# Kernel tuning notes

Measured on AMD Instinct MI355X. Metric: run time of the kernel, lower is better.

Reference implementation:

```python
import jax, jax.numpy as jnp
import numpy as np

B, T, D = 2, 2048, 2048   # batch, seq, model dim
H = 1408                  # expert hidden dim
E = 16                    # routed experts
S = 2                     # shared experts
TOP_K = 2
SCALE = 0.02


def setup_inputs() -> dict:
    key = jax.random.key(0)
    ks = jax.random.split(key, 6)
    return {
        "x": jax.random.normal(ks[0], (B, T, D), jnp.float32),
        "gate_w": jax.random.normal(ks[1], (D, E), jnp.float32) * SCALE,
        "shared_w1": jax.random.normal(ks[2], (S, D, H), jnp.float32) * SCALE,
        "shared_w2": jax.random.normal(ks[3], (S, H, D), jnp.float32) * SCALE,
        "expert_w1": jax.random.normal(ks[4], (E, D, H), jnp.float32) * SCALE,
        "expert_w2": jax.random.normal(ks[5], (E, H, D), jnp.float32) * SCALE,
    }


def reference(x, gate_w, shared_w1, shared_w2, expert_w1, expert_w2):
    xf = x.reshape(-1, x.shape[-1])            # [T_tot, D]
    n_tok = xf.shape[0]

    # shared experts: sum of SiLU FFNs
    sh = jax.nn.silu(jnp.einsum('td,sdh->sth', xf, shared_w1))
    shared_out = jnp.einsum('sth,shd->td', sh, shared_w2)

    # router
    logits = xf @ gate_w                       # [T_tot, E]
    probs = jax.nn.softmax(logits, axis=-1)
    topk_w, topk_idx = jax.lax.top_k(probs, TOP_K)
    topk_w = topk_w / topk_w.sum(axis=-1, keepdims=True)

    # aux load-balancing loss
    aux_loss = (probs.mean(axis=0) * logits.mean(axis=0)).sum() * E

    # scatter normalized top-k weights into dense [T_tot, E] combine matrix
    combine = jnp.zeros((n_tok, E), xf.dtype).at[
        jnp.arange(n_tok)[:, None], topk_idx
    ].add(topk_w)

    # routed experts computed densely over all tokens, combined by routing weights
    h = jax.nn.silu(jnp.einsum('td,edh->eth', xf, expert_w1))   # [E, T_tot, H]
    eo = jnp.einsum('eth,ehd->etd', h, expert_w2)               # [E, T_tot, D]
    routed_out = jnp.einsum('te,etd->td', combine, eo)

    total = (shared_out + routed_out).reshape(x.shape)
    return total, aux_loss
```

## Files before the change

kernel.cpp:

```cpp
#include <hip/hip_runtime.h>
#include <hip/hip_bf16.h>


#define T_TOT   4096
#define DMODEL  2048
#define HDIM    1408
#define NEXP    16
#define MAXSLOT 10240
#define MAXTILE 80

typedef short     bf16x8_t  __attribute__((ext_vector_type(8)));
typedef float     f32x4_t   __attribute__((ext_vector_type(4)));
typedef ushort    u16x8_t   __attribute__((ext_vector_type(8)));

__device__ __forceinline__ ushort f2bf(float f) {
    unsigned u = __float_as_uint(f);
    u += 0x7fffu + ((u >> 16) & 1u);
    return (ushort)(u >> 16);
}
__device__ __forceinline__ float bf2f(ushort b) { return __uint_as_float((unsigned)b << 16); }
__device__ __forceinline__ float silu(float v) { return v / (1.0f + __expf(-v)); }

__device__ __forceinline__ void async16(const ushort* g, ushort* l) {
    __builtin_amdgcn_global_load_lds((const __attribute__((address_space(1))) void*)g,
                                     (__attribute__((address_space(3))) void*)l, 16, 0, 0);
}


__global__ void init_kernel(int* cnt, double* ps, double* ls) {
    if (threadIdx.x < NEXP) { cnt[threadIdx.x] = 0; ps[threadIdx.x] = 0.0; ls[threadIdx.x] = 0.0; }
}

__global__ __launch_bounds__(256) void cvt_bf16(const float* __restrict__ src, ushort* __restrict__ dst) {
    size_t i = ((size_t)blockIdx.x * 256 + threadIdx.x) * 4;
    float4 v = *(const float4*)(src + i);
    ushort4 o; o.x = f2bf(v.x); o.y = f2bf(v.y); o.z = f2bf(v.z); o.w = f2bf(v.w);
    *(ushort4*)(dst + i) = o;
}

__global__ __launch_bounds__(256) void transpose_cvt(const float* __restrict__ src, ushort* __restrict__ dst,
                                                     int R, int C, long sbatch, long dbatch, int ldd) {
    __shared__ ushort t[64][72];
    const float* s = src + (long)blockIdx.z * sbatch;
    ushort* d = dst + (long)blockIdx.z * dbatch;
    int c0 = blockIdx.x * 64, r0 = blockIdx.y * 64;
    int tx = threadIdx.x & 15, ty = threadIdx.x >> 4;
#pragma unroll
    for (int i = 0; i < 4; i++) {
        int r = ty + i * 16;
        float4 v = *(const float4*)(s + (size_t)(r0 + r) * C + c0 + tx * 4);
        ushort4 o; o.x = f2bf(v.x); o.y = f2bf(v.y); o.z = f2bf(v.z); o.w = f2bf(v.w);
        *(ushort4*)&t[r][tx * 4] = o;
    }
    __syncthreads();
    int cx = threadIdx.x & 7, cy = threadIdx.x >> 3;
#pragma unroll
    for (int i = 0; i < 2; i++) {
        int cc = cy + i * 32;
        u16x8_t o;
#pragma unroll
        for (int j = 0; j < 8; j++) o[j] = t[cx * 8 + j][cc];
        *(u16x8_t*)(d + (size_t)(c0 + cc) * ldd + r0 + cx * 8) = o;
    }
}


__global__ __launch_bounds__(256) void router_kernel(const float* __restrict__ x, const float* __restrict__ gw,
                                                     int* __restrict__ topk_idx, float* __restrict__ topk_w,
                                                     double* __restrict__ probs_sum, double* __restrict__ logits_sum,
                                                     int* __restrict__ cnt) {
    const int wv = threadIdx.x >> 6, l = threadIdx.x & 63;
    const int tBase = blockIdx.x * 8 + wv * 2;

    float acc0[NEXP], acc1[NEXP];
#pragma unroll
    for (int e = 0; e < NEXP; e++) { acc0[e] = 0.f; acc1[e] = 0.f; }

    const float* x0 = x + (size_t)tBase * DMODEL;
    const float* x1 = x0 + DMODEL;

#pragma unroll
    for (int i = 0; i < 8; i++) {
        const int d0 = i * 256 + l * 4;
        float4 xa = *(const float4*)(x0 + d0);
        float4 xb = *(const float4*)(x1 + d0);
        const float4* g = (const float4*)(gw + (size_t)d0 * NEXP);
        float gf[64];
#pragma unroll
        for (int j = 0; j < 16; j++) {
            float4 t = g[j];
            gf[4 * j] = t.x; gf[4 * j + 1] = t.y; gf[4 * j + 2] = t.z; gf[4 * j + 3] = t.w;
        }
        const float xs0[4] = {xa.x, xa.y, xa.z, xa.w};
        const float xs1[4] = {xb.x, xb.y, xb.z, xb.w};
#pragma unroll
        for (int r = 0; r < 4; r++)
#pragma unroll
            for (int e = 0; e < NEXP; e++) {
                acc0[e] += xs0[r] * gf[r * 16 + e];
                acc1[e] += xs1[r] * gf[r * 16 + e];
            }
    }

#pragma unroll
    for (int e = 0; e < NEXP; e++) {
        acc0[e] += __shfl_xor(acc0[e], 32); acc0[e] += __shfl_xor(acc0[e], 16);
        acc1[e] += __shfl_xor(acc1[e], 32); acc1[e] += __shfl_xor(acc1[e], 16);
    }

    __shared__ float  sred[4][2][16][17];
    __shared__ double sp[4][2][NEXP], sl[4][2][NEXP];

    if (l < 16) {
#pragma unroll
        for (int e = 0; e < NEXP; e++) { sred[wv][0][l][e] = acc0[e]; sred[wv][1][l][e] = acc1[e]; }
    }
    __syncthreads();

    if (l < 32) {
        const int tok = l >> 4, e = l & 15;
        double lg = 0.0;
#pragma unroll
        for (int g = 0; g < 16; g++) lg += (double)sred[wv][tok][g][e];

        double m = lg;
#pragma unroll
        for (int off = 8; off; off >>= 1) { double o = __shfl_xor(m, off); m = o > m ? o : m; }
        double pe = exp(lg - m);
        double ss = pe;
#pragma unroll
        for (int off = 8; off; off >>= 1) ss += __shfl_xor(ss, off);
        double p = pe / ss;

        double v = p; int ie = e;
#pragma unroll
        for (int off = 8; off; off >>= 1) {
            double ov = __shfl_xor(v, off); int oi = __shfl_xor(ie, off);
            if (ov > v || (ov == v && oi < ie)) { v = ov; ie = oi; }
        }
        double v2 = (e == ie) ? -1.0 : p; int ie2 = e;
#pragma unroll
        for (int off = 8; off; off >>= 1) {
            double ov = __shfl_xor(v2, off); int oi = __shfl_xor(ie2, off);
            if (ov > v2 || (ov == v2 && oi < ie2)) { v2 = ov; ie2 = oi; }
        }

        sp[wv][tok][e] = p; sl[wv][tok][e] = lg;

        if (e == 0) {
            int t = tBase + tok;
            double s2 = v + v2;
            topk_idx[t * 2] = ie;  topk_idx[t * 2 + 1] = ie2;
            topk_w[t * 2] = (float)(v / s2); topk_w[t * 2 + 1] = (float)(v2 / s2);
            atomicAdd(&cnt[ie], 1); atomicAdd(&cnt[ie2], 1);
        }
    }
    __syncthreads();

    if (threadIdx.x < NEXP) {
        int e = threadIdx.x;
        double ps = 0.0, ls = 0.0;
#pragma unroll
        for (int w = 0; w < 4; w++) { ps += sp[w][0][e] + sp[w][1][e]; ls += sl[w][0][e] + sl[w][1][e]; }
        atomicAdd(&probs_sum[e], ps); atomicAdd(&logits_sum[e], ls);
    }
}

__global__ void setup_kernel(const int* __restrict__ cnt, int* __restrict__ cursor,
                             int* __restrict__ tile_expert, int* __restrict__ tile_row, int* __restrict__ meta,
                             int* __restrict__ slot_token, float* __restrict__ slot_w,
                             const double* __restrict__ probs_sum, const double* __restrict__ logits_sum,
                             float* __restrict__ out_aux) {
    if (threadIdx.x == 0) {
        int off = 0, nt = 0;
        for (int e = 0; e < NEXP; e++) {
            cursor[e] = off;
            int tiles = (cnt[e] + 127) >> 7;
            for (int j = 0; j < tiles; j++) { tile_expert[nt] = e; tile_row[nt] = off + j * 128; nt++; }
            off += tiles * 128;
        }
        meta[0] = nt; meta[1] = off;
        double aux = 0.0;
        for (int e = 0; e < NEXP; e++)
            aux += (probs_sum[e] / (double)T_TOT) * (logits_sum[e] / (double)T_TOT);
        out_aux[0] = (float)(aux * (double)NEXP);
    }
    __syncthreads();
    for (int i = threadIdx.x; i < MAXSLOT; i += 256) { slot_token[i] = 0; slot_w[i] = 0.0f; }
}

__global__ void scatter_kernel(const int* __restrict__ topk_idx, const float* __restrict__ topk_w,
                               int* __restrict__ cursor, int* __restrict__ slot_token, float* __restrict__ slot_w,
                               int* __restrict__ slot_of) {
    int t = blockIdx.x * 256 + threadIdx.x;
#pragma unroll
    for (int k = 0; k < 2; k++) {
        int e = topk_idx[t * 2 + k];
        int pos = atomicAdd(&cursor[e], 1);
        slot_token[pos] = t;
        slot_w[pos] = topk_w[t * 2 + k];
        slot_of[t * 2 + k] = pos;
    }
}


template<bool INDIRECT_A>
__device__ __forceinline__ void gemm_tile_core(const ushort* __restrict__ A, const ushort* __restrict__ B,
                                               int lda, int ldb, int K, int m0, int n0,
                                               const int* __restrict__ rowmap,
                                               f32x4_t acc[4][4], ushort* lds) {
    const int tid = threadIdx.x;
    const int w = tid >> 6, l = tid & 63;
    const int c0 = w * 2, c1 = c0 + 1;
    const int subrow = l >> 2;
    const int kc = (l & 3) * 8;
    int ar0 = c0 * 16 + subrow, ar1 = c1 * 16 + subrow;
    long ga0, ga1;
    if (INDIRECT_A) { ga0 = (long)rowmap[m0 + ar0]; ga1 = (long)rowmap[m0 + ar1]; }
    else            { ga0 = (long)(m0 + ar0);       ga1 = (long)(m0 + ar1); }
    const ushort* pa0 = A + ga0 * lda + kc;
    const ushort* pa1 = A + ga1 * lda + kc;
    const ushort* pb0 = B + (long)(n0 + ar0) * ldb + kc;
    const ushort* pb1 = B + (long)(n0 + ar1) * ldb + kc;
    const int wm = w & 1, wn = w >> 1;
    const int lrow = l & 15, quad = l >> 4;

    {
        ushort* d0 = lds + c0 * 512;
        ushort* d1 = lds + c1 * 512;
        async16(pa0, d0); async16(pa1, d1);
        async16(pb0, d0 + 4096); async16(pb1, d1 + 4096);
    }
    int cur = 0;
    for (int kt = 0; kt < K; kt += 32) {
        __syncthreads();
        if (kt + 32 < K) {
            pa0 += 32; pa1 += 32; pb0 += 32; pb1 += 32;
            ushort* e0 = lds + (cur ^ 1) * 8192 + c0 * 512;
            ushort* e1 = lds + (cur ^ 1) * 8192 + c1 * 512;
            async16(pa0, e0); async16(pa1, e1);
            async16(pb0, e0 + 4096); async16(pb1, e1 + 4096);
        }
        const ushort* As = lds + cur * 8192;
        const ushort* Bs = As + 4096;
        bf16x8_t a[4], b[4];
#pragma unroll
        for (int mi = 0; mi < 4; mi++)
            a[mi] = *(const bf16x8_t*)(As + (wm * 64 + mi * 16 + lrow) * 32 + quad * 8);
#pragma unroll
        for (int ni = 0; ni < 4; ni++)
            b[ni] = *(const bf16x8_t*)(Bs + (wn * 64 + ni * 16 + lrow) * 32 + quad * 8);
#pragma unroll
        for (int mi = 0; mi < 4; mi++)
#pragma unroll
            for (int ni = 0; ni < 4; ni++)
                acc[mi][ni] = __builtin_amdgcn_mfma_f32_16x16x32_bf16(a[mi], b[ni], acc[mi][ni], 0, 0, 0);
        cur ^= 1;
    }
}

template<int MODE>
__global__ __launch_bounds__(256, 3) void gemm_dense(const ushort* __restrict__ A, const ushort* __restrict__ B,
                                                     void* __restrict__ C, int lda, int ldb, int ldc, int K,
                                                     long bStride, int cZOff) {
    __shared__ ushort lds[16384];
    int m0 = blockIdx.x * 128, n0 = blockIdx.y * 128;
    const ushort* Bz = B + (long)blockIdx.z * bStride;
    f32x4_t acc[4][4];
#pragma unroll
    for (int mi = 0; mi < 4; mi++)
#pragma unroll
        for (int ni = 0; ni < 4; ni++) acc[mi][ni] = (f32x4_t){0.f, 0.f, 0.f, 0.f};
    gemm_tile_core<false>(A, Bz, lda, ldb, K, m0, n0, nullptr, acc, lds);

    const int w = threadIdx.x >> 6, l = threadIdx.x & 63;
    const int wm = w & 1, wn = w >> 1, quad = l >> 4, lcol = l & 15;
    int colBase = (int)blockIdx.z * cZOff + n0 + wn * 64;
#pragma unroll
    for (int mi = 0; mi < 4; mi++) {
        int rowb = m0 + wm * 64 + mi * 16 + quad * 4;
#pragma unroll
        for (int ni = 0; ni < 4; ni++) {
            int col = colBase + ni * 16 + lcol;
#pragma unroll
            for (int r = 0; r < 4; r++) {
                float v = acc[mi][ni][r];
                if (MODE == 0) ((ushort*)C)[(long)(rowb + r) * ldc + col] = f2bf(silu(v));
                else           ((float*)C)[(long)(rowb + r) * ldc + col] = v;
            }
        }
    }
}

template<int MODE>
__global__ __launch_bounds__(256, 3) void gemm_grouped(const ushort* __restrict__ A, const ushort* __restrict__ B,
                                                       void* __restrict__ C, int lda, int ldb, int ldc, int K,
                                                       long bExpertStride,
                                                       const int* __restrict__ tile_expert,
                                                       const int* __restrict__ tile_row,
                                                       const int* __restrict__ meta,
                                                       const int* __restrict__ slot_token,
                                                       const float* __restrict__ slot_w) {
    if ((int)blockIdx.x >= meta[0]) return;
    __shared__ ushort lds[16384];
    int e = tile_expert[blockIdx.x];
    int m0 = tile_row[blockIdx.x];
    int n0 = blockIdx.y * 128;
    const ushort* Be = B + (long)e * bExpertStride;
    f32x4_t acc[4][4];
#pragma unroll
    for (int mi = 0; mi < 4; mi++)
#pragma unroll
        for (int ni = 0; ni < 4; ni++) acc[mi][ni] = (f32x4_t){0.f, 0.f, 0.f, 0.f};
    gemm_tile_core<MODE == 1>(A, Be, lda, ldb, K, m0, n0, slot_token, acc, lds);

    const int w = threadIdx.x >> 6, l = threadIdx.x & 63;
    const int wm = w & 1, wn = w >> 1, quad = l >> 4, lcol = l & 15;
#pragma unroll
    for (int mi = 0; mi < 4; mi++) {
        int rowb = m0 + wm * 64 + mi * 16 + quad * 4;
#pragma unroll
        for (int ni = 0; ni < 4; ni++) {
            int col = n0 + wn * 64 + ni * 16 + lcol;
#pragma unroll
            for (int r = 0; r < 4; r++) {
                float v = acc[mi][ni][r];
                int row = rowb + r;
                if (MODE == 1) {
                    ((ushort*)C)[(long)row * ldc + col] = f2bf(silu(v));
                } else {
                    float wt = slot_w[row];
                    ((ushort*)C)[(long)row * ldc + col] = f2bf(v * wt);
                }
            }
        }
    }
}

__global__ __launch_bounds__(256) void combine_kernel(float* __restrict__ out, const ushort* __restrict__ ro,
                                                      const int* __restrict__ slot_of) {
    int t = blockIdx.x;
    int s1 = slot_of[t * 2], s2 = slot_of[t * 2 + 1];
    const u16x8_t* r1 = (const u16x8_t*)(ro + (size_t)s1 * DMODEL);
    const u16x8_t* r2 = (const u16x8_t*)(ro + (size_t)s2 * DMODEL);
    int i = threadIdx.x;
    u16x8_t a = r1[i], b = r2[i];
    float4* o = (float4*)(out + (size_t)t * DMODEL) + i * 2;
    float4 o0 = o[0], o1 = o[1];
    o0.x += bf2f(a[0]) + bf2f(b[0]); o0.y += bf2f(a[1]) + bf2f(b[1]);
    o0.z += bf2f(a[2]) + bf2f(b[2]); o0.w += bf2f(a[3]) + bf2f(b[3]);
    o1.x += bf2f(a[4]) + bf2f(b[4]); o1.y += bf2f(a[5]) + bf2f(b[5]);
    o1.z += bf2f(a[6]) + bf2f(b[6]); o1.w += bf2f(a[7]) + bf2f(b[7]);
    o[0] = o0; o[1] = o1;
}


extern "C" void kernel_launch(void* const* d_in, const int* in_sizes, int n_in,
                              void* d_out, int out_size, void* d_ws, size_t ws_size,
                              hipStream_t stream) {
    const float* x   = (const float*)d_in[0];
    const float* gw  = (const float*)d_in[1];
    const float* sw1 = (const float*)d_in[2];
    const float* sw2 = (const float*)d_in[3];
    const float* ew1 = (const float*)d_in[4];
    const float* ew2 = (const float*)d_in[5];
    float* out = (float*)d_out;

    char* p = (char*)d_ws;
    auto alloc = [&](size_t bytes) { char* r = p; p += (bytes + 511) & ~(size_t)511; return r; };
    ushort* xb    = (ushort*)alloc((size_t)T_TOT * DMODEL * 2);
    ushort* w1t   = (ushort*)alloc((size_t)2 * HDIM * DMODEL * 2);
    ushort* w2t   = (ushort*)alloc((size_t)DMODEL * 2 * HDIM * 2);
    ushort* ew1t  = (ushort*)alloc((size_t)NEXP * HDIM * DMODEL * 2);
    ushort* ew2t  = (ushort*)alloc((size_t)NEXP * DMODEL * HDIM * 2);
    ushort* h     = (ushort*)alloc((size_t)T_TOT * 2 * HDIM * 2);
    ushort* hg    = (ushort*)alloc((size_t)MAXSLOT * HDIM * 2);
    ushort* ro    = (ushort*)alloc((size_t)MAXSLOT * DMODEL * 2);
    int*    slot_token = (int*)alloc(MAXSLOT * 4);
    float*  slot_w     = (float*)alloc(MAXSLOT * 4);
    int*    slot_of    = (int*)alloc(T_TOT * 2 * 4);
    int*    topk_idx   = (int*)alloc(T_TOT * 2 * 4);
    float*  topk_w     = (float*)alloc(T_TOT * 2 * 4);
    int*    cnt        = (int*)alloc(64);
    int*    cursor     = (int*)alloc(64);
    int*    tile_expert= (int*)alloc(512);
    int*    tile_row   = (int*)alloc(512);
    int*    meta       = (int*)alloc(64);
    double* probs_sum  = (double*)alloc(128);
    double* logits_sum = (double*)alloc(128);

    init_kernel<<<1, 64, 0, stream>>>(cnt, probs_sum, logits_sum);
    cvt_bf16<<<(T_TOT * DMODEL) / 1024, 256, 0, stream>>>(x, xb);
    transpose_cvt<<<dim3(HDIM / 64, DMODEL / 64, 2), 256, 0, stream>>>(
        sw1, w1t, DMODEL, HDIM, (long)DMODEL * HDIM, (long)HDIM * DMODEL, DMODEL);
    transpose_cvt<<<dim3(DMODEL / 64, HDIM / 64, 2), 256, 0, stream>>>(
        sw2, w2t, HDIM, DMODEL, (long)HDIM * DMODEL, (long)HDIM, 2 * HDIM);
    transpose_cvt<<<dim3(HDIM / 64, DMODEL / 64, NEXP), 256, 0, stream>>>(
        ew1, ew1t, DMODEL, HDIM, (long)DMODEL * HDIM, (long)HDIM * DMODEL, DMODEL);
    transpose_cvt<<<dim3(DMODEL / 64, HDIM / 64, NEXP), 256, 0, stream>>>(
        ew2, ew2t, HDIM, DMODEL, (long)HDIM * DMODEL, (long)DMODEL * HDIM, HDIM);

    router_kernel<<<T_TOT / 8, 256, 0, stream>>>(x, gw, topk_idx, topk_w, probs_sum, logits_sum, cnt);
    setup_kernel<<<1, 256, 0, stream>>>(cnt, cursor, tile_expert, tile_row, meta,
                                        slot_token, slot_w, probs_sum, logits_sum, out + (size_t)T_TOT * DMODEL);
    scatter_kernel<<<T_TOT / 256, 256, 0, stream>>>(topk_idx, topk_w, cursor, slot_token, slot_w, slot_of);

    gemm_dense<0><<<dim3(T_TOT / 128, HDIM / 128, 2), 256, 0, stream>>>(
        xb, w1t, h, DMODEL, DMODEL, 2 * HDIM, DMODEL, (long)HDIM * DMODEL, HDIM);
    gemm_grouped<1><<<dim3(MAXTILE, HDIM / 128), 256, 0, stream>>>(
        xb, ew1t, hg, DMODEL, DMODEL, HDIM, DMODEL, (long)HDIM * DMODEL,
        tile_expert, tile_row, meta, slot_token, slot_w);
    gemm_dense<2><<<dim3(T_TOT / 128, DMODEL / 128, 1), 256, 0, stream>>>(
        h, w2t, out, 2 * HDIM, 2 * HDIM, DMODEL, 2 * HDIM, 0L, 0);
    gemm_grouped<3><<<dim3(MAXTILE, DMODEL / 128), 256, 0, stream>>>(
        hg, ew2t, ro, HDIM, HDIM, DMODEL, HDIM, (long)DMODEL * HDIM,
        tile_expert, tile_row, meta, slot_token, slot_w);
    combine_kernel<<<T_TOT, 256, 0, stream>>>(out, ro, slot_of);
}
```

Measured before the change: 914.0 us.

## Merge prep, routing-plan and GEMM launches into fewer combined kernels

Collapses the conversion, transpose, router, setup and scatter kernels into one prep kernel plus a single-block plan kernel. The x-to-bf16 conversion is folded into the router, and router statistics are written as per-block partials instead of global atomics. The dense shared-expert GEMM and the grouped expert GEMM are merged into one launch per layer, so both run in the same grid and fill the GPU better. This saves launch overhead and tail idle time, but adds a serial single-block plan step that handles histogram, zeroing and scatter.

```diff
diff --git a/kernel.cpp b/kernel.cpp
--- a/kernel.cpp
+++ b/kernel.cpp
@@ -8,6 +8,7 @@
 #define NEXP    16
 #define MAXSLOT 10240
 #define MAXTILE 80
+#define RBLK    512
 
 typedef short     bf16x8_t  __attribute__((ext_vector_type(8)));
 typedef float     f32x4_t   __attribute__((ext_vector_type(4)));
@@ -27,30 +28,30 @@
 }
 
 
-__global__ void init_kernel(int* cnt, double* ps, double* ls) {
-    if (threadIdx.x < NEXP) { cnt[threadIdx.x] = 0; ps[threadIdx.x] = 0.0; ls[threadIdx.x] = 0.0; }
-}
-
-__global__ __launch_bounds__(256) void cvt_bf16(const float* __restrict__ src, ushort* __restrict__ dst) {
-    size_t i = ((size_t)blockIdx.x * 256 + threadIdx.x) * 4;
-    float4 v = *(const float4*)(src + i);
-    ushort4 o; o.x = f2bf(v.x); o.y = f2bf(v.y); o.z = f2bf(v.z); o.w = f2bf(v.w);
-    *(ushort4*)(dst + i) = o;
-}
-
-__global__ __launch_bounds__(256) void transpose_cvt(const float* __restrict__ src, ushort* __restrict__ dst,
-                                                     int R, int C, long sbatch, long dbatch, int ldd) {
-    __shared__ ushort t[64][72];
-    const float* s = src + (long)blockIdx.z * sbatch;
-    ushort* d = dst + (long)blockIdx.z * dbatch;
-    int c0 = blockIdx.x * 64, r0 = blockIdx.y * 64;
+union SMem {
+    struct {
+        float  sred[4][2][16][17];
+        double sp[4][2][NEXP];
+        double sl[4][2][NEXP];
+    } r;
+    ushort t[64][72];
+};
+
+__device__ __forceinline__ void transpose_tile(SMem& sm, int id,
+        const float* __restrict__ src, ushort* __restrict__ dst,
+        int C, long sbatch, long dbatch, int ldd, int TX, int TY) {
+    int z = id / (TX * TY); int rem = id - z * TX * TY;
+    int bx = rem % TX, by = rem / TX;
+    const float* s = src + (long)z * sbatch;
+    ushort* d = dst + (long)z * dbatch;
+    int c0 = bx * 64, r0 = by * 64;
     int tx = threadIdx.x & 15, ty = threadIdx.x >> 4;
 #pragma unroll
     for (int i = 0; i < 4; i++) {
         int r = ty + i * 16;
         float4 v = *(const float4*)(s + (size_t)(r0 + r) * C + c0 + tx * 4);
         ushort4 o; o.x = f2bf(v.x); o.y = f2bf(v.y); o.z = f2bf(v.z); o.w = f2bf(v.w);
-        *(ushort4*)&t[r][tx * 4] = o;
+        *(ushort4*)&sm.t[r][tx * 4] = o;
     }
     __syncthreads();
     int cx = threadIdx.x & 7, cy = threadIdx.x >> 3;
@@ -59,18 +60,17 @@
         int cc = cy + i * 32;
         u16x8_t o;
 #pragma unroll
-        for (int j = 0; j < 8; j++) o[j] = t[cx * 8 + j][cc];
+        for (int j = 0; j < 8; j++) o[j] = sm.t[cx * 8 + j][cc];
         *(u16x8_t*)(d + (size_t)(c0 + cc) * ldd + r0 + cx * 8) = o;
     }
 }
 
-
-__global__ __launch_bounds__(256) void router_kernel(const float* __restrict__ x, const float* __restrict__ gw,
-                                                     int* __restrict__ topk_idx, float* __restrict__ topk_w,
-                                                     double* __restrict__ probs_sum, double* __restrict__ logits_sum,
-                                                     int* __restrict__ cnt) {
+__device__ __forceinline__ void router_block(SMem& sm, int bid,
+        const float* __restrict__ x, const float* __restrict__ gw, ushort* __restrict__ xbuf,
+        int* __restrict__ topk_idx, float* __restrict__ topk_w,
+        double* __restrict__ pparts, double* __restrict__ lparts) {
     const int wv = threadIdx.x >> 6, l = threadIdx.x & 63;
-    const int tBase = blockIdx.x * 8 + wv * 2;
+    const int tBase = bid * 8 + wv * 2;
 
     float acc0[NEXP], acc1[NEXP];
 #pragma unroll
@@ -78,28 +78,32 @@
 
     const float* x0 = x + (size_t)tBase * DMODEL;
     const float* x1 = x0 + DMODEL;
+    ushort* xo0 = xbuf + (size_t)tBase * DMODEL;
+    ushort* xo1 = xo0 + DMODEL;
 
 #pragma unroll
     for (int i = 0; i < 8; i++) {
         const int d0 = i * 256 + l * 4;
         float4 xa = *(const float4*)(x0 + d0);
-        float4 xb = *(const float4*)(x1 + d0);
-        const float4* g = (const float4*)(gw + (size_t)d0 * NEXP);
-        float gf[64];
-#pragma unroll
-        for (int j = 0; j < 16; j++) {
-            float4 t = g[j];
-            gf[4 * j] = t.x; gf[4 * j + 1] = t.y; gf[4 * j + 2] = t.z; gf[4 * j + 3] = t.w;
-        }
+        float4 xb4 = *(const float4*)(x1 + d0);
+        ushort4 oa; oa.x = f2bf(xa.x); oa.y = f2bf(xa.y); oa.z = f2bf(xa.z); oa.w = f2bf(xa.w);
+        ushort4 ob; ob.x = f2bf(xb4.x); ob.y = f2bf(xb4.y); ob.z = f2bf(xb4.z); ob.w = f2bf(xb4.w);
+        *(ushort4*)(xo0 + d0) = oa;
+        *(ushort4*)(xo1 + d0) = ob;
         const float xs0[4] = {xa.x, xa.y, xa.z, xa.w};
-        const float xs1[4] = {xb.x, xb.y, xb.z, xb.w};
-#pragma unroll
-        for (int r = 0; r < 4; r++)
+        const float xs1[4] = {xb4.x, xb4.y, xb4.z, xb4.w};
+#pragma unroll
+        for (int r = 0; r < 4; r++) {
+            const float4* g = (const float4*)(gw + (size_t)(d0 + r) * NEXP);
+            float4 q0 = g[0], q1 = g[1], q2 = g[2], q3 = g[3];
+            const float gf[16] = {q0.x, q0.y, q0.z, q0.w, q1.x, q1.y, q1.z, q1.w,
+                                  q2.x, q2.y, q2.z, q2.w, q3.x, q3.y, q3.z, q3.w};
 #pragma unroll
             for (int e = 0; e < NEXP; e++) {
-                acc0[e] += xs0[r] * gf[r * 16 + e];
-                acc1[e] += xs1[r] * gf[r * 16 + e];
+                acc0[e] += xs0[r] * gf[e];
+                acc1[e] += xs1[r] * gf[e];
             }
+        }
     }
 
 #pragma unroll
@@ -108,12 +112,9 @@
         acc1[e] += __shfl_xor(acc1[e], 32); acc1[e] += __shfl_xor(acc1[e], 16);
     }
 
-    __shared__ float  sred[4][2][16][17];
-    __shared__ double sp[4][2][NEXP], sl[4][2][NEXP];
-
     if (l < 16) {
 #pragma unroll
-        for (int e = 0; e < NEXP; e++) { sred[wv][0][l][e] = acc0[e]; sred[wv][1][l][e] = acc1[e]; }
+        for (int e = 0; e < NEXP; e++) { sm.r.sred[wv][0][l][e] = acc0[e]; sm.r.sred[wv][1][l][e] = acc1[e]; }
     }
     __syncthreads();
 
@@ -121,7 +122,7 @@
         const int tok = l >> 4, e = l & 15;
         double lg = 0.0;
 #pragma unroll
-        for (int g = 0; g < 16; g++) lg += (double)sred[wv][tok][g][e];
+        for (int g = 0; g < 16; g++) lg += (double)sm.r.sred[wv][tok][g][e];
 
         double m = lg;
 #pragma unroll
@@ -145,14 +146,13 @@
             if (ov > v2 || (ov == v2 && oi < ie2)) { v2 = ov; ie2 = oi; }
         }
 
-        sp[wv][tok][e] = p; sl[wv][tok][e] = lg;
+        sm.r.sp[wv][tok][e] = p; sm.r.sl[wv][tok][e] = lg;
 
         if (e == 0) {
             int t = tBase + tok;
             double s2 = v + v2;
             topk_idx[t * 2] = ie;  topk_idx[t * 2 + 1] = ie2;
             topk_w[t * 2] = (float)(v / s2); topk_w[t * 2 + 1] = (float)(v2 / s2);
-            atomicAdd(&cnt[ie], 1); atomicAdd(&cnt[ie2], 1);
         }
     }
     __syncthreads();
@@ -161,45 +161,95 @@
         int e = threadIdx.x;
         double ps = 0.0, ls = 0.0;
 #pragma unroll
-        for (int w = 0; w < 4; w++) { ps += sp[w][0][e] + sp[w][1][e]; ls += sl[w][0][e] + sl[w][1][e]; }
-        atomicAdd(&probs_sum[e], ps); atomicAdd(&logits_sum[e], ls);
-    }
-}
-
-__global__ void setup_kernel(const int* __restrict__ cnt, int* __restrict__ cursor,
-                             int* __restrict__ tile_expert, int* __restrict__ tile_row, int* __restrict__ meta,
-                             int* __restrict__ slot_token, float* __restrict__ slot_w,
-                             const double* __restrict__ probs_sum, const double* __restrict__ logits_sum,
-                             float* __restrict__ out_aux) {
-    if (threadIdx.x == 0) {
+        for (int w = 0; w < 4; w++) { ps += sm.r.sp[w][0][e] + sm.r.sp[w][1][e]; ls += sm.r.sl[w][0][e] + sm.r.sl[w][1][e]; }
+        pparts[bid * NEXP + e] = ps;
+        lparts[bid * NEXP + e] = ls;
+    }
+}
+
+#define PB0 RBLK
+#define PB1 (PB0 + 1408)
+#define PB2 (PB1 + 1408)
+#define PB3 (PB2 + 11264)
+#define PB4 (PB3 + 11264)
+
+__global__ __launch_bounds__(256) void prep_kernel(
+        const float* __restrict__ x, const float* __restrict__ gw,
+        const float* __restrict__ sw1, const float* __restrict__ sw2,
+        const float* __restrict__ ew1, const float* __restrict__ ew2,
+        ushort* __restrict__ xb, ushort* __restrict__ w1t, ushort* __restrict__ w2t,
+        ushort* __restrict__ ew1t, ushort* __restrict__ ew2t,
+        int* __restrict__ topk_idx, float* __restrict__ topk_w,
+        double* __restrict__ pparts, double* __restrict__ lparts) {
+    __shared__ SMem sm;
+    int bid = blockIdx.x;
+    if (bid < PB0) {
+        router_block(sm, bid, x, gw, xb, topk_idx, topk_w, pparts, lparts);
+    } else if (bid < PB1) {
+        transpose_tile(sm, bid - PB0, sw1, w1t, HDIM, (long)DMODEL * HDIM, (long)HDIM * DMODEL,
+                       DMODEL, HDIM / 64, DMODEL / 64);
+    } else if (bid < PB2) {
+        transpose_tile(sm, bid - PB1, sw2, w2t, DMODEL, (long)HDIM * DMODEL, (long)HDIM,
+                       2 * HDIM, DMODEL / 64, HDIM / 64);
+    } else if (bid < PB3) {
+        transpose_tile(sm, bid - PB2, ew1, ew1t, HDIM, (long)DMODEL * HDIM, (long)HDIM * DMODEL,
+                       DMODEL, HDIM / 64, DMODEL / 64);
+    } else {
+        transpose_tile(sm, bid - PB3, ew2, ew2t, DMODEL, (long)HDIM * DMODEL, (long)DMODEL * HDIM,
+                       HDIM, DMODEL / 64, HDIM / 64);
+    }
+}
+
+
+__global__ __launch_bounds__(1024) void plan_kernel(
+        const int* __restrict__ topk_idx, const float* __restrict__ topk_w,
+        const double* __restrict__ pparts, const double* __restrict__ lparts,
+        int* __restrict__ tile_expert, int* __restrict__ tile_row, int* __restrict__ meta,
+        int* __restrict__ slot_token, float* __restrict__ slot_w, int* __restrict__ slot_of,
+        float* __restrict__ out_aux) {
+    __shared__ int hist[NEXP];
+    __shared__ int curs[NEXP];
+    __shared__ double pred[32][NEXP], lred[32][NEXP];
+    __shared__ double paux[NEXP], laux[NEXP];
+    const int tid = threadIdx.x;
+    if (tid < NEXP) hist[tid] = 0;
+    __syncthreads();
+    for (int i = tid; i < T_TOT * 2; i += 1024) atomicAdd(&hist[topk_idx[i]], 1);
+    for (int i = tid; i < MAXSLOT; i += 1024) { slot_token[i] = 0; slot_w[i] = 0.0f; }
+    if (tid < 512) {
+        int e = tid & 15, c = tid >> 4;
+        double ps = 0.0, ls = 0.0;
+        for (int b = c * 16; b < c * 16 + 16; b++) { ps += pparts[b * NEXP + e]; ls += lparts[b * NEXP + e]; }
+        pred[c][e] = ps; lred[c][e] = ls;
+    }
+    __syncthreads();
+    if (tid < NEXP) {
+        double ps = 0.0, ls = 0.0;
+        for (int c = 0; c < 32; c++) { ps += pred[c][tid]; ls += lred[c][tid]; }
+        paux[tid] = ps; laux[tid] = ls;
+    }
+    __syncthreads();
+    if (tid == 0) {
         int off = 0, nt = 0;
         for (int e = 0; e < NEXP; e++) {
-            cursor[e] = off;
-            int tiles = (cnt[e] + 127) >> 7;
+            curs[e] = off;
+            int tiles = (hist[e] + 127) >> 7;
             for (int j = 0; j < tiles; j++) { tile_expert[nt] = e; tile_row[nt] = off + j * 128; nt++; }
             off += tiles * 128;
         }
         meta[0] = nt; meta[1] = off;
         double aux = 0.0;
         for (int e = 0; e < NEXP; e++)
-            aux += (probs_sum[e] / (double)T_TOT) * (logits_sum[e] / (double)T_TOT);
+            aux += (paux[e] / (double)T_TOT) * (laux[e] / (double)T_TOT);
         out_aux[0] = (float)(aux * (double)NEXP);
     }
     __syncthreads();
-    for (int i = threadIdx.x; i < MAXSLOT; i += 256) { slot_token[i] = 0; slot_w[i] = 0.0f; }
-}
-
-__global__ void scatter_kernel(const int* __restrict__ topk_idx, const float* __restrict__ topk_w,
-                               int* __restrict__ cursor, int* __restrict__ slot_token, float* __restrict__ slot_w,
-                               int* __restrict__ slot_of) {
-    int t = blockIdx.x * 256 + threadIdx.x;
-#pragma unroll
-    for (int k = 0; k < 2; k++) {
-        int e = topk_idx[t * 2 + k];
-        int pos = atomicAdd(&cursor[e], 1);
-        slot_token[pos] = t;
-        slot_w[pos] = topk_w[t * 2 + k];
-        slot_of[t * 2 + k] = pos;
+    for (int i = tid; i < T_TOT * 2; i += 1024) {
+        int e = topk_idx[i];
+        int pos = atomicAdd(&curs[e], 1);
+        slot_token[pos] = i >> 1;
+        slot_w[pos] = topk_w[i];
+        slot_of[i] = pos;
     }
 }
 
@@ -259,78 +309,98 @@
     }
 }
 
-template<int MODE>
-__global__ __launch_bounds__(256, 3) void gemm_dense(const ushort* __restrict__ A, const ushort* __restrict__ B,
-                                                     void* __restrict__ C, int lda, int ldb, int ldc, int K,
-                                                     long bStride, int cZOff) {
+__global__ __launch_bounds__(256, 3) void gemm_p1(const ushort* __restrict__ xb,
+        const ushort* __restrict__ w1t, const ushort* __restrict__ ew1t,
+        ushort* __restrict__ h, ushort* __restrict__ hg,
+        const int* __restrict__ tile_expert, const int* __restrict__ tile_row,
+        const int* __restrict__ meta, const int* __restrict__ slot_token) {
     __shared__ ushort lds[16384];
-    int m0 = blockIdx.x * 128, n0 = blockIdx.y * 128;
-    const ushort* Bz = B + (long)blockIdx.z * bStride;
     f32x4_t acc[4][4];
 #pragma unroll
     for (int mi = 0; mi < 4; mi++)
 #pragma unroll
         for (int ni = 0; ni < 4; ni++) acc[mi][ni] = (f32x4_t){0.f, 0.f, 0.f, 0.f};
-    gemm_tile_core<false>(A, Bz, lda, ldb, K, m0, n0, nullptr, acc, lds);
+
+    const int bid = blockIdx.x;
+    ushort* C; int ldc, m0, n0, colBase;
+    if (bid < 704) {
+        int z = bid / 352, rem = bid % 352;
+        m0 = (rem % 32) * 128; n0 = (rem / 32) * 128;
+        gemm_tile_core<false>(xb, w1t + (long)z * HDIM * DMODEL, DMODEL, DMODEL, DMODEL,
+                              m0, n0, nullptr, acc, lds);
+        C = h; ldc = 2 * HDIM; colBase = z * HDIM + n0;
+    } else {
+        int r = bid - 704;
+        int tile = r % MAXTILE; n0 = (r / MAXTILE) * 128;
+        if (tile >= meta[0]) return;
+        int e = tile_expert[tile]; m0 = tile_row[tile];
+        gemm_tile_core<true>(xb, ew1t + (long)e * HDIM * DMODEL, DMODEL, DMODEL, DMODEL,
+                             m0, n0, slot_token, acc, lds);
+        C = hg; ldc = HDIM; colBase = n0;
+    }
 
     const int w = threadIdx.x >> 6, l = threadIdx.x & 63;
     const int wm = w & 1, wn = w >> 1, quad = l >> 4, lcol = l & 15;
-    int colBase = (int)blockIdx.z * cZOff + n0 + wn * 64;
 #pragma unroll
     for (int mi = 0; mi < 4; mi++) {
         int rowb = m0 + wm * 64 + mi * 16 + quad * 4;
 #pragma unroll
         for (int ni = 0; ni < 4; ni++) {
-            int col = colBase + ni * 16 + lcol;
-#pragma unroll
-            for (int r = 0; r < 4; r++) {
-                float v = acc[mi][ni][r];
-                if (MODE == 0) ((ushort*)C)[(long)(rowb + r) * ldc + col] = f2bf(silu(v));
-                else           ((float*)C)[(long)(rowb + r) * ldc + col] = v;
-            }
-        }
-    }
-}
-
-template<int MODE>
-__global__ __launch_bounds__(256, 3) void gemm_grouped(const ushort* __restrict__ A, const ushort* __restrict__ B,
-                                                       void* __restrict__ C, int lda, int ldb, int ldc, int K,
-                                                       long bExpertStride,
-                                                       const int* __restrict__ tile_expert,
-                                                       const int* __restrict__ tile_row,
-                                                       const int* __restrict__ meta,
-                                                       const int* __restrict__ slot_token,
-                                                       const float* __restrict__ slot_w) {
-    if ((int)blockIdx.x >= meta[0]) return;
+            int col = colBase + wn * 64 + ni * 16 + lcol;
+#pragma unroll
+            for (int r = 0; r < 4; r++)
+                C[(long)(rowb + r) * ldc + col] = f2bf(silu(acc[mi][ni][r]));
+        }
+    }
+}
+
+__global__ __launch_bounds__(256, 3) void gemm_p2(const ushort* __restrict__ h,
+        const ushort* __restrict__ w2t, const ushort* __restrict__ hg, const ushort* __restrict__ ew2t,
+        float* __restrict__ out, ushort* __restrict__ ro,
+        const int* __restrict__ tile_expert, const int* __restrict__ tile_row,
+        const int* __restrict__ meta, const float* __restrict__ slot_w) {
     __shared__ ushort lds[16384];
-    int e = tile_expert[blockIdx.x];
-    int m0 = tile_row[blockIdx.x];
-    int n0 = blockIdx.y * 128;
-    const ushort* Be = B + (long)e * bExpertStride;
     f32x4_t acc[4][4];
 #pragma unroll
     for (int mi = 0; mi < 4; mi++)
 #pragma unroll
         for (int ni = 0; ni < 4; ni++) acc[mi][ni] = (f32x4_t){0.f, 0.f, 0.f, 0.f};
-    gemm_tile_core<MODE == 1>(A, Be, lda, ldb, K, m0, n0, slot_token, acc, lds);
-
+
+    const int bid = blockIdx.x;
     const int w = threadIdx.x >> 6, l = threadIdx.x & 63;
     const int wm = w & 1, wn = w >> 1, quad = l >> 4, lcol = l & 15;
-#pragma unroll
-    for (int mi = 0; mi < 4; mi++) {
-        int rowb = m0 + wm * 64 + mi * 16 + quad * 4;
-#pragma unroll
-        for (int ni = 0; ni < 4; ni++) {
-            int col = n0 + wn * 64 + ni * 16 + lcol;
-#pragma unroll
-            for (int r = 0; r < 4; r++) {
-                float v = acc[mi][ni][r];
-                int row = rowb + r;
-                if (MODE == 1) {
-                    ((ushort*)C)[(long)row * ldc + col] = f2bf(silu(v));
-                } else {
-                    float wt = slot_w[row];
-                    ((ushort*)C)[(long)row * ldc + col] = f2bf(v * wt);
+
+    if (bid < 512) {
+        int m0 = (bid % 32) * 128, n0 = (bid / 32) * 128;
+        gemm_tile_core<false>(h, w2t, 2 * HDIM, 2 * HDIM, 2 * HDIM, m0, n0, nullptr, acc, lds);
+#pragma unroll
+        for (int mi = 0; mi < 4; mi++) {
+            int rowb = m0 + wm * 64 + mi * 16 + quad * 4;
+#pragma unroll
+            for (int ni = 0; ni < 4; ni++) {
+                int col = n0 + wn * 64 + ni * 16 + lcol;
+#pragma unroll
+                for (int r = 0; r < 4; r++)
+                    out[(long)(rowb + r) * DMODEL + col] = acc[mi][ni][r];
+            }
+        }
+    } else {
+        int r0 = bid - 512;
+        int tile = r0 % MAXTILE; int n0 = (r0 / MAXTILE) * 128;
+        if (tile >= meta[0]) return;
+        int e = tile_expert[tile]; int m0 = tile_row[tile];
+        gemm_tile_core<false>(hg, ew2t + (long)e * DMODEL * HDIM, HDIM, HDIM, HDIM,
+                              m0, n0, nullptr, acc, lds);
+#pragma unroll
+        for (int mi = 0; mi < 4; mi++) {
+            int rowb = m0 + wm * 64 + mi * 16 + quad * 4;
+#pragma unroll
+            for (int ni = 0; ni < 4; ni++) {
+                int col = n0 + wn * 64 + ni * 16 + lcol;
+#pragma unroll
+                for (int r = 0; r < 4; r++) {
+                    int row = rowb + r;
+                    ro[(long)row * DMODEL + col] = f2bf(acc[mi][ni][r] * slot_w[row]);
                 }
             }
         }
@@ -381,39 +451,21 @@
     int*    slot_of    = (int*)alloc(T_TOT * 2 * 4);
     int*    topk_idx   = (int*)alloc(T_TOT * 2 * 4);
     float*  topk_w     = (float*)alloc(T_TOT * 2 * 4);
-    int*    cnt        = (int*)alloc(64);
-    int*    cursor     = (int*)alloc(64);
     int*    tile_expert= (int*)alloc(512);
     int*    tile_row   = (int*)alloc(512);
     int*    meta       = (int*)alloc(64);
-    double* probs_sum  = (double*)alloc(128);
-    double* logits_sum = (double*)alloc(128);
-
-    init_kernel<<<1, 64, 0, stream>>>(cnt, probs_sum, logits_sum);
-    cvt_bf16<<<(T_TOT * DMODEL) / 1024, 256, 0, stream>>>(x, xb);
-    transpose_cvt<<<dim3(HDIM / 64, DMODEL / 64, 2), 256, 0, stream>>>(
-        sw1, w1t, DMODEL, HDIM, (long)DMODEL * HDIM, (long)HDIM * DMODEL, DMODEL);
-    transpose_cvt<<<dim3(DMODEL / 64, HDIM / 64, 2), 256, 0, stream>>>(
-        sw2, w2t, HDIM, DMODEL, (long)HDIM * DMODEL, (long)HDIM, 2 * HDIM);
-    transpose_cvt<<<dim3(HDIM / 64, DMODEL / 64, NEXP), 256, 0, stream>>>(
-        ew1, ew1t, DMODEL, HDIM, (long)DMODEL * HDIM, (long)HDIM * DMODEL, DMODEL);
-    transpose_cvt<<<dim3(DMODEL / 64, HDIM / 64, NEXP), 256, 0, stream>>>(
-        ew2, ew2t, HDIM, DMODEL, (long)HDIM * DMODEL, (long)DMODEL * HDIM, HDIM);
-
-    router_kernel<<<T_TOT / 8, 256, 0, stream>>>(x, gw, topk_idx, topk_w, probs_sum, logits_sum, cnt);
-    setup_kernel<<<1, 256, 0, stream>>>(cnt, cursor, tile_expert, tile_row, meta,
-                                        slot_token, slot_w, probs_sum, logits_sum, out + (size_t)T_TOT * DMODEL);
-    scatter_kernel<<<T_TOT / 256, 256, 0, stream>>>(topk_idx, topk_w, cursor, slot_token, slot_w, slot_of);
-
-    gemm_dense<0><<<dim3(T_TOT / 128, HDIM / 128, 2), 256, 0, stream>>>(
-        xb, w1t, h, DMODEL, DMODEL, 2 * HDIM, DMODEL, (long)HDIM * DMODEL, HDIM);
-    gemm_grouped<1><<<dim3(MAXTILE, HDIM / 128), 256, 0, stream>>>(
-        xb, ew1t, hg, DMODEL, DMODEL, HDIM, DMODEL, (long)HDIM * DMODEL,
-        tile_expert, tile_row, meta, slot_token, slot_w);
-    gemm_dense<2><<<dim3(T_TOT / 128, DMODEL / 128, 1), 256, 0, stream>>>(
-        h, w2t, out, 2 * HDIM, 2 * HDIM, DMODEL, 2 * HDIM, 0L, 0);
-    gemm_grouped<3><<<dim3(MAXTILE, DMODEL / 128), 256, 0, stream>>>(
-        hg, ew2t, ro, HDIM, HDIM, DMODEL, HDIM, (long)DMODEL * HDIM,
-        tile_expert, tile_row, meta, slot_token, slot_w);
+    double* pparts     = (double*)alloc((size_t)RBLK * NEXP * 8);
+    double* lparts     = (double*)alloc((size_t)RBLK * NEXP * 8);
+
+    prep_kernel<<<PB4, 256, 0, stream>>>(x, gw, sw1, sw2, ew1, ew2,
+                                         xb, w1t, w2t, ew1t, ew2t,
+                                         topk_idx, topk_w, pparts, lparts);
+    plan_kernel<<<1, 1024, 0, stream>>>(topk_idx, topk_w, pparts, lparts,
+                                        tile_expert, tile_row, meta,
+                                        slot_token, slot_w, slot_of, out + (size_t)T_TOT * DMODEL);
+    gemm_p1<<<704 + MAXTILE * (HDIM / 128), 256, 0, stream>>>(
+        xb, w1t, ew1t, h, hg, tile_expert, tile_row, meta, slot_token);
+    gemm_p2<<<512 + MAXTILE * (DMODEL / 128), 256, 0, stream>>>(
+        h, w2t, hg, ew2t, out, ro, tile_expert, tile_row, meta, slot_w);
     combine_kernel<<<T_TOT, 256, 0, stream>>>(out, ro, slot_of);
 }
```

New measurement: 811.0 us. 1.13x faster.
